# Kernel tuning notes

Measured on AMD Instinct MI355X. Metric: run time of the kernel, lower is better.

The kernel has to match this reference:

```python
import jax, jax.numpy as jnp
import numpy as np

N_NODES = 100000
N_EDGES = 625000
D = 128


def setup_inputs() -> dict:
    key = jax.random.key(0)
    ks = jax.random.split(key, 6)
    x = jax.random.normal(ks[0], (N_NODES, D), dtype=jnp.float32)
    src = jax.random.randint(ks[1], (N_EDGES,), 0, N_NODES, dtype=jnp.int32)
    dst = jnp.sort(jax.random.randint(ks[2], (N_EDGES,), 0, N_NODES, dtype=jnp.int32))
    edge_w = jax.random.uniform(ks[3], (N_EDGES,), dtype=jnp.float32)
    # linear layer params (fan-in scaled)
    W = jax.random.normal(ks[4], (D, D), dtype=jnp.float32) / np.sqrt(D)
    b = jnp.zeros((D,), dtype=jnp.float32)
    # highway gate params (glorot-uniform-ish range as in source)
    init_range = np.sqrt(2.0 / (D + D)).astype(np.float32)
    kernel_gate = jax.random.uniform(ks[5], (D, D), dtype=jnp.float32,
                                     minval=-init_range, maxval=init_range)
    bias_gate = jnp.zeros((D,), dtype=jnp.float32)
    return {"x": x, "src": src, "dst": dst, "edge_w": edge_w,
            "W": W, "b": b, "kernel_gate": kernel_gate, "bias_gate": bias_gate}


def reference(x, src, dst, edge_w, W, b, kernel_gate, bias_gate):
    # hidden = Linear(x); dropout is identity in eval mode
    hidden = x @ W.T + b                                  # [N, D]
    # support = spmm(adj, hidden): gather src rows, weight, scatter-add to dst
    msgs = edge_w[:, None] * hidden[src]                  # [E, D]
    support = jax.ops.segment_sum(msgs, dst, num_segments=x.shape[0])
    support = jax.nn.relu(support)                        # act
    # highway gate
    gate = jax.nn.sigmoid(x @ kernel_gate + bias_gate)    # [N, D]
    out = gate * support + (1.0 - gate) * x
    return out
```

## Files before the change

kernel.cpp:

```cpp
#include <hip/hip_runtime.h>

#define DD 128

typedef __attribute__((ext_vector_type(8))) short bf16x8;
typedef __attribute__((ext_vector_type(4))) float f32x4;

__device__ __forceinline__ unsigned int cvt_pk_bf16(float lo, float hi) {
  unsigned int r;
  asm("v_cvt_pk_bf16_f32 %0, %1, %2" : "=v"(r) : "v"(lo), "v"(hi));
  return r;
}
__device__ __forceinline__ float bf_lo(unsigned int v) { return __uint_as_float(v << 16); }
__device__ __forceinline__ float bf_hi(unsigned int v) { return __uint_as_float(v & 0xFFFF0000u); }

__global__ __launch_bounds__(256) void prep_kernel(
    const float* __restrict__ x, const int* __restrict__ dst,
    const float* __restrict__ W, const float* __restrict__ KG,
    unsigned char* __restrict__ xq, float* __restrict__ sx,
    int* __restrict__ row_start, unsigned short* __restrict__ B,
    int N, int E, int ABLK, int BBLK) {
  int blk = blockIdx.x;
  int t = threadIdx.x;
  if (blk < ABLK) {
    int n = blk * 16 + (t >> 4);
    int lr = t & 15;
    if (n < N) {
      const float4* xr = (const float4*)(x + (size_t)n * DD);
      float4 va = xr[lr * 2], vb = xr[lr * 2 + 1];
      float m = fmaxf(fmaxf(fmaxf(fabsf(va.x), fabsf(va.y)), fmaxf(fabsf(va.z), fabsf(va.w))),
                      fmaxf(fmaxf(fabsf(vb.x), fabsf(vb.y)), fmaxf(fabsf(vb.z), fabsf(vb.w))));
#pragma unroll
      for (int d = 1; d < 16; d <<= 1) m = fmaxf(m, __shfl_xor(m, d, 16));
      m = fmaxf(m, 1e-20f);
      float inv = 127.0f / m;
      unsigned int q0 = (unsigned int)(__float2int_rn(va.x * inv) + 128);
      unsigned int q1 = (unsigned int)(__float2int_rn(va.y * inv) + 128);
      unsigned int q2 = (unsigned int)(__float2int_rn(va.z * inv) + 128);
      unsigned int q3 = (unsigned int)(__float2int_rn(va.w * inv) + 128);
      unsigned int q4 = (unsigned int)(__float2int_rn(vb.x * inv) + 128);
      unsigned int q5 = (unsigned int)(__float2int_rn(vb.y * inv) + 128);
      unsigned int q6 = (unsigned int)(__float2int_rn(vb.z * inv) + 128);
      unsigned int q7 = (unsigned int)(__float2int_rn(vb.w * inv) + 128);
      uint2 qp;
      qp.x = q0 | (q1 << 8) | (q2 << 16) | (q3 << 24);
      qp.y = q4 | (q5 << 8) | (q6 << 16) | (q7 << 24);
      ((uint2*)xq)[(size_t)n * 16 + lr] = qp;
      if (lr == 0) sx[n] = m * (1.0f / 127.0f);
    }
  } else if (blk < ABLK + BBLK) {
    int e = (blk - ABLK) * 256 + t;
    if (e <= E) {
      if (e == 0) {
        int d0 = dst[0];
        for (int n = 0; n <= d0; ++n) row_start[n] = 0;
      } else if (e == E) {
        for (int n = dst[E - 1] + 1; n <= N; ++n) row_start[n] = E;
      } else {
        int d = dst[e], dp = dst[e - 1];
        for (int n = dp + 1; n <= d; ++n) row_start[n] = e;
      }
    }
  } else {
    int e2 = (blk - ABLK - BBLK) * 256 + t;
    if (e2 < 2 * DD * DD) {
      int j = e2 >> 7, k = e2 & 127;
      float v = (j < DD) ? W[j * DD + k] : KG[k * DD + (j - DD)];
      B[e2] = (unsigned short)cvt_pk_bf16(v, v);
    }
  }
}

__global__ __launch_bounds__(256, 8) void scatter_agg(
    const unsigned char* __restrict__ xq, const float* __restrict__ sx,
    const int* __restrict__ src, const float* __restrict__ ew,
    const int* __restrict__ row_start, unsigned short* __restrict__ aggb,
    float* __restrict__ sumw, int N, int E) {
  int t = threadIdx.x;
  int wid = t >> 6, lane = t & 63;
  int g = lane >> 4, lr = lane & 15;
  int n = blockIdx.x * 16 + wid * 4 + g;
  bool valid = (n < N);
  int b = valid ? row_start[n] : 0;
  int cnt = valid ? (row_start[n + 1] - b) : 0;
  const uint2* x8 = (const uint2*)xq;

  float a[8];
#pragma unroll
  for (int k = 0; k < 8; ++k) a[k] = 0.f;
  float wsum = 0.f, wsc = 0.f;
  int clampj = cnt > 0 ? cnt - 1 : 0;

  int i = 0;
  while (__any(i < cnt)) {
#pragma unroll
    for (int u = 0; u < 4; ++u) {
      int ii = i + u;
      int jj = ii < clampj ? ii : clampj;
      int j = b + jj;
      if (j > E - 1) j = E - 1;
      float wt = (ii < cnt) ? ew[j] : 0.f;
      int s = src[j];
      float ws = wt * sx[s];
      uint2 v = x8[(size_t)s * 16 + lr];
      wsum += wt;
      wsc += ws;
      a[0] += ws * (float)(v.x & 0xFF);
      a[1] += ws * (float)((v.x >> 8) & 0xFF);
      a[2] += ws * (float)((v.x >> 16) & 0xFF);
      a[3] += ws * (float)(v.x >> 24);
      a[4] += ws * (float)(v.y & 0xFF);
      a[5] += ws * (float)((v.y >> 8) & 0xFF);
      a[6] += ws * (float)((v.y >> 16) & 0xFF);
      a[7] += ws * (float)(v.y >> 24);
    }
    i += 4;
  }
  float c = 128.0f * wsc;
#pragma unroll
  for (int k = 0; k < 8; ++k) a[k] -= c;

  if (valid) {
    uint4 o;
    o.x = cvt_pk_bf16(a[0], a[1]);
    o.y = cvt_pk_bf16(a[2], a[3]);
    o.z = cvt_pk_bf16(a[4], a[5]);
    o.w = cvt_pk_bf16(a[6], a[7]);
    ((uint4*)aggb)[(size_t)n * 16 + lr] = o;
    if (lr == 0) sumw[n] = wsum;
  }
}

__global__ __launch_bounds__(256, 4) void fused_gemm(
    const unsigned char* __restrict__ xq, const float* __restrict__ sx,
    const unsigned short* __restrict__ aggb, const unsigned short* __restrict__ B,
    const float* __restrict__ sumw, const float* __restrict__ bias,
    const float* __restrict__ bg, float* __restrict__ out, int N) {
  __shared__ char smem[16 * 1024];
  unsigned short* sX = (unsigned short*)smem;
  int t = threadIdx.x;
  int wid = t >> 6, lane = t & 63;
  int lr = lane & 15, lk2 = lane >> 4;
  int jw = wid * 32;
  int M0 = blockIdx.x * 64;

#pragma unroll
  for (int i = 0; i < 2; ++i) {
    int idx = i * 256 + t;
    int r = idx >> 3;
    int c = idx & 7;
    uint4 v;
    float s;
    if (M0 + r < N) {
      v = ((const uint4*)(xq + (size_t)(M0 + r) * DD))[c];
      s = sx[M0 + r];
    } else {
      v = make_uint4(0, 0, 0, 0);
      s = 0.f;
    }
    float nb = -128.0f * s;
    unsigned int w[4] = {v.x, v.y, v.z, v.w};
    unsigned int o[8];
#pragma unroll
    for (int q = 0; q < 4; ++q) {
      float e0 = fmaf(s, (float)(w[q] & 0xFF), nb);
      float e1 = fmaf(s, (float)((w[q] >> 8) & 0xFF), nb);
      float e2 = fmaf(s, (float)((w[q] >> 16) & 0xFF), nb);
      float e3 = fmaf(s, (float)(w[q] >> 24), nb);
      o[q * 2]     = cvt_pk_bf16(e0, e1);
      o[q * 2 + 1] = cvt_pk_bf16(e2, e3);
    }
    int base = r * 256 + c * 32;
    uint4 lo = {o[0], o[1], o[2], o[3]};
    uint4 hi = {o[4], o[5], o[6], o[7]};
    *(uint4*)((char*)sX + ((base) ^ ((r & 7) << 4)))      = lo;
    *(uint4*)((char*)sX + ((base + 16) ^ ((r & 7) << 4))) = hi;
  }
  __syncthreads();

  const unsigned short* arow[4];
#pragma unroll
  for (int nr = 0; nr < 4; ++nr) {
    int node = M0 + nr * 16 + lr;
    if (node > N - 1) node = N - 1;
    arow[nr] = aggb + (size_t)node * DD;
  }

  f32x4 accS[2][4], accG[2][4];
#pragma unroll
  for (int m = 0; m < 2; ++m)
#pragma unroll
    for (int nr = 0; nr < 4; ++nr) {
      accS[m][nr] = (f32x4){0.f, 0.f, 0.f, 0.f};
      accG[m][nr] = (f32x4){0.f, 0.f, 0.f, 0.f};
    }

#pragma unroll
  for (int kc = 0; kc < 4; ++kc) {
    int kb = (kc * 32 + lk2 * 8) * 2;
    bf16x8 wSk[2], wGk[2];
#pragma unroll
    for (int m = 0; m < 2; ++m) {
      int j = jw + m * 16 + lr;
      wSk[m] = *(const bf16x8*)(B + (size_t)j * DD + kc * 32 + lk2 * 8);
      wGk[m] = *(const bf16x8*)(B + (size_t)(DD + j) * DD + kc * 32 + lk2 * 8);
    }
    bf16x8 af[4], xf[4];
#pragma unroll
    for (int nr = 0; nr < 4; ++nr) {
      af[nr] = *(const bf16x8*)(arow[nr] + kc * 32 + lk2 * 8);
      int r = nr * 16 + lr;
      xf[nr] = *(const bf16x8*)((const char*)sX + ((r * 256 + kb) ^ ((r & 7) << 4)));
    }
#pragma unroll
    for (int m = 0; m < 2; ++m)
#pragma unroll
      for (int nr = 0; nr < 4; ++nr) {
        accS[m][nr] = __builtin_amdgcn_mfma_f32_16x16x32_bf16(wSk[m], af[nr], accS[m][nr], 0, 0, 0);
        accG[m][nr] = __builtin_amdgcn_mfma_f32_16x16x32_bf16(wGk[m], xf[nr], accG[m][nr], 0, 0, 0);
      }
  }

#pragma unroll
  for (int m = 0; m < 2; ++m) {
    int j0 = jw + m * 16 + lk2 * 4;
    float4 b4 = *(const float4*)&bias[j0];
    float4 bg4 = *(const float4*)&bg[j0];
    float ba[4] = {b4.x, b4.y, b4.z, b4.w};
    float bga[4] = {bg4.x, bg4.y, bg4.z, bg4.w};
#pragma unroll
    for (int nr = 0; nr < 4; ++nr) {
      int node = M0 + nr * 16 + lr;
      if (node < N) {
        float sw = sumw[node];
        int r = nr * 16 + lr;
        uint2 qx = *(const uint2*)((const char*)sX + ((r * 256 + j0 * 2) ^ ((r & 7) << 4)));
        float xr[4] = {bf_lo(qx.x), bf_hi(qx.x), bf_lo(qx.y), bf_hi(qx.y)};
        f32x4 vs = accS[m][nr], vg = accG[m][nr];
        float4 o;
        float* op = &o.x;
#pragma unroll
        for (int reg = 0; reg < 4; ++reg) {
          float s = fmaxf(vs[reg] + sw * ba[reg], 0.f);
          float g = 1.0f / (1.0f + __expf(-(vg[reg] + bga[reg])));
          op[reg] = g * s + (1.0f - g) * xr[reg];
        }
        *(float4*)&out[(size_t)node * DD + j0] = o;
      }
    }
  }
}

extern "C" void kernel_launch(void* const* d_in, const int* in_sizes, int n_in,
                              void* d_out, int out_size, void* d_ws, size_t ws_size,
                              hipStream_t stream) {
  const float* x   = (const float*)d_in[0];
  const int*   src = (const int*)d_in[1];
  const int*   dst = (const int*)d_in[2];
  const float* ew  = (const float*)d_in[3];
  const float* W   = (const float*)d_in[4];
  const float* b   = (const float*)d_in[5];
  const float* KG  = (const float*)d_in[6];
  const float* bg  = (const float*)d_in[7];
  float* out = (float*)d_out;

  int N = in_sizes[0] / DD;
  int E = in_sizes[1];

  unsigned short* aggb = (unsigned short*)d_ws;
  unsigned char* xq = (unsigned char*)(aggb + (size_t)N * DD);
  float* sx = (float*)(xq + (size_t)N * DD);
  float* sumw = sx + N;
  unsigned short* B = (unsigned short*)(sumw + N);
  int* row_start = (int*)(B + 2 * DD * DD);

  int ABLK = (N + 15) / 16;
  int BBLK = (E + 1 + 255) / 256;
  int CBLK = (2 * DD * DD + 255) / 256;
  prep_kernel<<<ABLK + BBLK + CBLK, 256, 0, stream>>>(x, dst, W, KG, xq, sx,
                                                      row_start, B, N, E, ABLK, BBLK);
  scatter_agg<<<(N + 15) / 16, 256, 0, stream>>>(xq, sx, src, ew, row_start, aggb, sumw, N, E);
  fused_gemm<<<(N + 63) / 64, 256, 0, stream>>>(xq, sx, aggb, B, sumw, b, bg, out, N);
}
```

Before: 83.12 us.

## Fuse scatter aggregation and dual GEMM into one kernel via shared memory

Merges the aggregation kernel and the fused GEMM kernel into one. Each 16-node block aggregates neighbour rows into shared memory, dequantizes its x rows into shared memory, then runs both MFMA GEMMs and the highway epilogue without a global round-trip. This removes the bf16 agg buffer write and read, the sumw buffer, and one kernel launch. The cost is smaller GEMM tiles (16 rows per block): each block reloads the full B weight matrix with less reuse, and the GEMM phase runs at lower occupancy.

After: 90.95 us. 9.4% more time.

```diff
diff --git a/kernel.cpp b/kernel.cpp
--- a/kernel.cpp
+++ b/kernel.cpp
@@ -70,15 +70,53 @@
   }
 }
 
-__global__ __launch_bounds__(256, 8) void scatter_agg(
+__global__ __launch_bounds__(256, 6) void agg_gemm(
     const unsigned char* __restrict__ xq, const float* __restrict__ sx,
     const int* __restrict__ src, const float* __restrict__ ew,
-    const int* __restrict__ row_start, unsigned short* __restrict__ aggb,
-    float* __restrict__ sumw, int N, int E) {
+    const int* __restrict__ row_start, const unsigned short* __restrict__ B,
+    const float* __restrict__ bias, const float* __restrict__ bg,
+    float* __restrict__ out, int N, int E) {
+  __shared__ char smem[8320];
+  unsigned short* sX = (unsigned short*)smem;
+  unsigned short* sA = (unsigned short*)(smem + 4096);
+  float* sumw_s = (float*)(smem + 8192);
   int t = threadIdx.x;
   int wid = t >> 6, lane = t & 63;
-  int g = lane >> 4, lr = lane & 15;
-  int n = blockIdx.x * 16 + wid * 4 + g;
+  int g = lane >> 4, lr = lane & 15, lk2 = lane >> 4;
+  int M0 = blockIdx.x * 16;
+
+  if (t < 128) {
+    int r = t >> 3, c = t & 7;
+    int n = M0 + r;
+    uint4 v;
+    float s;
+    if (n < N) {
+      v = ((const uint4*)(xq + (size_t)n * DD))[c];
+      s = sx[n];
+    } else {
+      v = make_uint4(0, 0, 0, 0);
+      s = 0.f;
+    }
+    float nb = -128.0f * s;
+    unsigned int w[4] = {v.x, v.y, v.z, v.w};
+    unsigned int o[8];
+#pragma unroll
+    for (int q = 0; q < 4; ++q) {
+      float e0 = fmaf(s, (float)(w[q] & 0xFF), nb);
+      float e1 = fmaf(s, (float)((w[q] >> 8) & 0xFF), nb);
+      float e2 = fmaf(s, (float)((w[q] >> 16) & 0xFF), nb);
+      float e3 = fmaf(s, (float)(w[q] >> 24), nb);
+      o[q * 2]     = cvt_pk_bf16(e0, e1);
+      o[q * 2 + 1] = cvt_pk_bf16(e2, e3);
+    }
+    int base = r * 256 + c * 32;
+    uint4 lo = {o[0], o[1], o[2], o[3]};
+    uint4 hi = {o[4], o[5], o[6], o[7]};
+    *(uint4*)((char*)sX + ((base) ^ ((r & 7) << 4)))      = lo;
+    *(uint4*)((char*)sX + ((base + 16) ^ ((r & 7) << 4))) = hi;
+  }
+
+  int n = M0 + wid * 4 + g;
   bool valid = (n < N);
   int b = valid ? row_start[n] : 0;
   int cnt = valid ? (row_start[n + 1] - b) : 0;
@@ -115,84 +153,28 @@
     }
     i += 4;
   }
-  float c = 128.0f * wsc;
-#pragma unroll
-  for (int k = 0; k < 8; ++k) a[k] -= c;
-
-  if (valid) {
+  float c0 = 128.0f * wsc;
+#pragma unroll
+  for (int k = 0; k < 8; ++k) a[k] -= c0;
+
+  {
+    int rt = wid * 4 + g;
     uint4 o;
     o.x = cvt_pk_bf16(a[0], a[1]);
     o.y = cvt_pk_bf16(a[2], a[3]);
     o.z = cvt_pk_bf16(a[4], a[5]);
     o.w = cvt_pk_bf16(a[6], a[7]);
-    ((uint4*)aggb)[(size_t)n * 16 + lr] = o;
-    if (lr == 0) sumw[n] = wsum;
-  }
-}
-
-__global__ __launch_bounds__(256, 4) void fused_gemm(
-    const unsigned char* __restrict__ xq, const float* __restrict__ sx,
-    const unsigned short* __restrict__ aggb, const unsigned short* __restrict__ B,
-    const float* __restrict__ sumw, const float* __restrict__ bias,
-    const float* __restrict__ bg, float* __restrict__ out, int N) {
-  __shared__ char smem[16 * 1024];
-  unsigned short* sX = (unsigned short*)smem;
-  int t = threadIdx.x;
-  int wid = t >> 6, lane = t & 63;
-  int lr = lane & 15, lk2 = lane >> 4;
-  int jw = wid * 32;
-  int M0 = blockIdx.x * 64;
-
-#pragma unroll
-  for (int i = 0; i < 2; ++i) {
-    int idx = i * 256 + t;
-    int r = idx >> 3;
-    int c = idx & 7;
-    uint4 v;
-    float s;
-    if (M0 + r < N) {
-      v = ((const uint4*)(xq + (size_t)(M0 + r) * DD))[c];
-      s = sx[M0 + r];
-    } else {
-      v = make_uint4(0, 0, 0, 0);
-      s = 0.f;
-    }
-    float nb = -128.0f * s;
-    unsigned int w[4] = {v.x, v.y, v.z, v.w};
-    unsigned int o[8];
-#pragma unroll
-    for (int q = 0; q < 4; ++q) {
-      float e0 = fmaf(s, (float)(w[q] & 0xFF), nb);
-      float e1 = fmaf(s, (float)((w[q] >> 8) & 0xFF), nb);
-      float e2 = fmaf(s, (float)((w[q] >> 16) & 0xFF), nb);
-      float e3 = fmaf(s, (float)(w[q] >> 24), nb);
-      o[q * 2]     = cvt_pk_bf16(e0, e1);
-      o[q * 2 + 1] = cvt_pk_bf16(e2, e3);
-    }
-    int base = r * 256 + c * 32;
-    uint4 lo = {o[0], o[1], o[2], o[3]};
-    uint4 hi = {o[4], o[5], o[6], o[7]};
-    *(uint4*)((char*)sX + ((base) ^ ((r & 7) << 4)))      = lo;
-    *(uint4*)((char*)sX + ((base + 16) ^ ((r & 7) << 4))) = hi;
+    *(uint4*)((char*)sA + ((rt * 256 + lr * 16) ^ ((rt & 7) << 4))) = o;
+    if (lr == 0) sumw_s[rt] = wsum;
   }
   __syncthreads();
 
-  const unsigned short* arow[4];
-#pragma unroll
-  for (int nr = 0; nr < 4; ++nr) {
-    int node = M0 + nr * 16 + lr;
-    if (node > N - 1) node = N - 1;
-    arow[nr] = aggb + (size_t)node * DD;
-  }
-
-  f32x4 accS[2][4], accG[2][4];
-#pragma unroll
-  for (int m = 0; m < 2; ++m)
-#pragma unroll
-    for (int nr = 0; nr < 4; ++nr) {
-      accS[m][nr] = (f32x4){0.f, 0.f, 0.f, 0.f};
-      accG[m][nr] = (f32x4){0.f, 0.f, 0.f, 0.f};
-    }
+  f32x4 accS[2], accG[2];
+#pragma unroll
+  for (int m = 0; m < 2; ++m) {
+    accS[m] = (f32x4){0.f, 0.f, 0.f, 0.f};
+    accG[m] = (f32x4){0.f, 0.f, 0.f, 0.f};
+  }
 
 #pragma unroll
   for (int kc = 0; kc < 4; ++kc) {
@@ -200,52 +182,41 @@
     bf16x8 wSk[2], wGk[2];
 #pragma unroll
     for (int m = 0; m < 2; ++m) {
-      int j = jw + m * 16 + lr;
+      int j = (wid * 2 + m) * 16 + lr;
       wSk[m] = *(const bf16x8*)(B + (size_t)j * DD + kc * 32 + lk2 * 8);
       wGk[m] = *(const bf16x8*)(B + (size_t)(DD + j) * DD + kc * 32 + lk2 * 8);
     }
-    bf16x8 af[4], xf[4];
-#pragma unroll
-    for (int nr = 0; nr < 4; ++nr) {
-      af[nr] = *(const bf16x8*)(arow[nr] + kc * 32 + lk2 * 8);
-      int r = nr * 16 + lr;
-      xf[nr] = *(const bf16x8*)((const char*)sX + ((r * 256 + kb) ^ ((r & 7) << 4)));
-    }
-#pragma unroll
-    for (int m = 0; m < 2; ++m)
-#pragma unroll
-      for (int nr = 0; nr < 4; ++nr) {
-        accS[m][nr] = __builtin_amdgcn_mfma_f32_16x16x32_bf16(wSk[m], af[nr], accS[m][nr], 0, 0, 0);
-        accG[m][nr] = __builtin_amdgcn_mfma_f32_16x16x32_bf16(wGk[m], xf[nr], accG[m][nr], 0, 0, 0);
+    bf16x8 af = *(const bf16x8*)((const char*)sA + ((lr * 256 + kb) ^ ((lr & 7) << 4)));
+    bf16x8 xf = *(const bf16x8*)((const char*)sX + ((lr * 256 + kb) ^ ((lr & 7) << 4)));
+#pragma unroll
+    for (int m = 0; m < 2; ++m) {
+      accS[m] = __builtin_amdgcn_mfma_f32_16x16x32_bf16(wSk[m], af, accS[m], 0, 0, 0);
+      accG[m] = __builtin_amdgcn_mfma_f32_16x16x32_bf16(wGk[m], xf, accG[m], 0, 0, 0);
+    }
+  }
+
+  int node = M0 + lr;
+  if (node < N) {
+    float sw = sumw_s[lr];
+#pragma unroll
+    for (int m = 0; m < 2; ++m) {
+      int j0 = (wid * 2 + m) * 16 + lk2 * 4;
+      float4 b4 = *(const float4*)&bias[j0];
+      float4 bg4 = *(const float4*)&bg[j0];
+      float ba[4] = {b4.x, b4.y, b4.z, b4.w};
+      float bga[4] = {bg4.x, bg4.y, bg4.z, bg4.w};
+      uint2 qx = *(const uint2*)((const char*)sX + ((lr * 256 + j0 * 2) ^ ((lr & 7) << 4)));
+      float xr[4] = {bf_lo(qx.x), bf_hi(qx.x), bf_lo(qx.y), bf_hi(qx.y)};
+      f32x4 vs = accS[m], vg = accG[m];
+      float4 o;
+      float* op = &o.x;
+#pragma unroll
+      for (int reg = 0; reg < 4; ++reg) {
+        float s = fmaxf(vs[reg] + sw * ba[reg], 0.f);
+        float gt = 1.0f / (1.0f + __expf(-(vg[reg] + bga[reg])));
+        op[reg] = gt * s + (1.0f - gt) * xr[reg];
       }
-  }
-
-#pragma unroll
-  for (int m = 0; m < 2; ++m) {
-    int j0 = jw + m * 16 + lk2 * 4;
-    float4 b4 = *(const float4*)&bias[j0];
-    float4 bg4 = *(const float4*)&bg[j0];
-    float ba[4] = {b4.x, b4.y, b4.z, b4.w};
-    float bga[4] = {bg4.x, bg4.y, bg4.z, bg4.w};
-#pragma unroll
-    for (int nr = 0; nr < 4; ++nr) {
-      int node = M0 + nr * 16 + lr;
-      if (node < N) {
-        float sw = sumw[node];
-        int r = nr * 16 + lr;
-        uint2 qx = *(const uint2*)((const char*)sX + ((r * 256 + j0 * 2) ^ ((r & 7) << 4)));
-        float xr[4] = {bf_lo(qx.x), bf_hi(qx.x), bf_lo(qx.y), bf_hi(qx.y)};
-        f32x4 vs = accS[m][nr], vg = accG[m][nr];
-        float4 o;
-        float* op = &o.x;
-#pragma unroll
-        for (int reg = 0; reg < 4; ++reg) {
-          float s = fmaxf(vs[reg] + sw * ba[reg], 0.f);
-          float g = 1.0f / (1.0f + __expf(-(vg[reg] + bga[reg])));
-          op[reg] = g * s + (1.0f - g) * xr[reg];
-        }
-        *(float4*)&out[(size_t)node * DD + j0] = o;
-      }
+      *(float4*)&out[(size_t)node * DD + j0] = o;
     }
   }
 }
@@ -266,11 +237,9 @@
   int N = in_sizes[0] / DD;
   int E = in_sizes[1];
 
-  unsigned short* aggb = (unsigned short*)d_ws;
-  unsigned char* xq = (unsigned char*)(aggb + (size_t)N * DD);
+  unsigned char* xq = (unsigned char*)d_ws;
   float* sx = (float*)(xq + (size_t)N * DD);
-  float* sumw = sx + N;
-  unsigned short* B = (unsigned short*)(sumw + N);
+  unsigned short* B = (unsigned short*)(sx + N);
   int* row_start = (int*)(B + 2 * DD * DD);
 
   int ABLK = (N + 15) / 16;
@@ -278,6 +247,5 @@
   int CBLK = (2 * DD * DD + 255) / 256;
   prep_kernel<<<ABLK + BBLK + CBLK, 256, 0, stream>>>(x, dst, W, KG, xq, sx,
                                                       row_start, B, N, E, ABLK, BBLK);
-  scatter_agg<<<(N + 15) / 16, 256, 0, stream>>>(xq, sx, src, ew, row_start, aggb, sumw, N, E);
-  fused_gemm<<<(N + 63) / 64, 256, 0, stream>>>(xq, sx, aggb, B, sumw, b, bg, out, N);
-}
+  agg_gemm<<<(N + 15) / 16, 256, 0, stream>>>(xq, sx, src, ew, row_start, B, b, bg, out, N, E);
+}
```
